# Performance work log

Hardware: AMD Instinct MI355X
Metric: run time of the kernel (lower is better)

The kernel has to match this reference:

```python
import jax, jax.numpy as jnp
import numpy as np

INPUT_DIM = 66
OUTPUT_COUNT = 8192
NUM_PAIRS = 65536

def setup_inputs() -> dict:
    key = jax.random.key(0)
    k1, k2, k3, k4 = jax.random.split(key, 4)
    x = jax.random.normal(k1, (NUM_PAIRS, INPUT_DIM), dtype=jnp.float32)
    query = jax.random.normal(k2, (OUTPUT_COUNT, INPUT_DIM), dtype=jnp.float32)
    # nn.Linear(input_dim, input_dim): weight [out,in], bias [out]
    bound = 1.0 / np.sqrt(INPUT_DIM)
    Wk = jax.random.uniform(k3, (INPUT_DIM, INPUT_DIM), minval=-bound, maxval=bound, dtype=jnp.float32)
    bk = jax.random.uniform(k4, (INPUT_DIM,), minval=-bound, maxval=bound, dtype=jnp.float32)
    return {"x": x, "query": query, "Wk": Wk, "bk": bk}

def reference(x, query, Wk, bk):
    # K = Linear(x): x @ Wk^T + bk  -> [num_pairs, d]
    K = x @ Wk.T + bk
    # scores: [output_count, num_pairs]
    scores = jnp.einsum("qd,nd->qn", query, K)
    attn = jax.nn.softmax(scores, axis=1)
    # selected: [output_count, d] — note values are raw x, not K
    selected = attn @ x
    return selected
```

## Files before the change

kernel.cpp:

```cpp
#include <hip/hip_runtime.h>
#include <cstdint>


typedef __bf16    bf16x4 __attribute__((ext_vector_type(4)));
typedef __bf16    bf16x8 __attribute__((ext_vector_type(8)));
typedef _Float16  f16x4  __attribute__((ext_vector_type(4)));
typedef _Float16  f16x8  __attribute__((ext_vector_type(8)));
typedef float     f32x16 __attribute__((ext_vector_type(16)));

extern "C" __device__ float __ocml_native_exp2_f32(float);

#define NUM_PAIRS   65536
#define NUM_Q       8192
#define DIM         66
#define KPITCH      84
#define QPITCH      80
#define XROWS       96
#define XPITCH      36
#define XTILE       (XROWS*XPITCH)
#define PARTP       68

#define LDS_XT 10752
#define STG    24576
#define KSTRIDE 10752
#define XSTRIDE 13824

__device__ __forceinline__ bf16x8 frag8(const __bf16* p) {
    bf16x4 lo = *(const bf16x4*)p;
    bf16x4 hi = *(const bf16x4*)(p + 4);
    return __builtin_shufflevector(lo, hi, 0, 1, 2, 3, 4, 5, 6, 7);
}
__device__ __forceinline__ f16x8 frag8h(const _Float16* p) {
    f16x4 lo = *(const f16x4*)p;
    f16x4 hi = *(const f16x4*)(p + 4);
    return __builtin_shufflevector(lo, hi, 0, 1, 2, 3, 4, 5, 6, 7);
}
__device__ __forceinline__ f32x16 mfma_bf16(bf16x8 a, bf16x8 b, f32x16 c) {
    return __builtin_amdgcn_mfma_f32_32x32x16_bf16(a, b, c, 0, 0, 0);
}
__device__ __forceinline__ f32x16 mfma_f16(f16x8 a, f16x8 b, f32x16 c) {
    return __builtin_amdgcn_mfma_f32_32x32x16_f16(a, b, c, 0, 0, 0);
}

__device__ __forceinline__ void plswap(unsigned &a, unsigned &b) {
    asm("v_permlane32_swap_b32 %0, %1" : "+v"(a), "+v"(b));
}
__device__ __forceinline__ unsigned packbf(float a, float b) {
    union { __bf16 h[2]; unsigned u; } t;
    t.h[0] = (__bf16)a; t.h[1] = (__bf16)b;
    return t.u;
}

union U4 { unsigned u[4]; bf16x8 v; };

__device__ __forceinline__ void makefrags(const f32x16 &s, U4 *f) {
    float P[16];
    #pragma unroll
    for (int r = 0; r < 16; ++r) P[r] = __ocml_native_exp2_f32(s[r]);
    unsigned E0 = packbf(P[0],  P[1]),  E1 = packbf(P[2],  P[3]);
    unsigned F0 = packbf(P[4],  P[5]),  F1 = packbf(P[6],  P[7]);
    plswap(E0, F0); plswap(E1, F1);
    f[0].u[0] = E0; f[0].u[1] = E1; f[0].u[2] = F0; f[0].u[3] = F1;
    unsigned G0 = packbf(P[8],  P[9]),  G1 = packbf(P[10], P[11]);
    unsigned H0 = packbf(P[12], P[13]), H1 = packbf(P[14], P[15]);
    plswap(G0, H0); plswap(G1, H1);
    f[1].u[0] = G0; f[1].u[1] = G1; f[1].u[2] = H0; f[1].u[3] = H1;
}

__device__ __forceinline__ void stage_tile(char* dst, const char* gK, const char* gX,
                                           int wave, int lane) {
    #pragma unroll
    for (int j = 0; j < 6; ++j) {
        int c = wave + 4 * j;
        int off = c * 1024 + lane * 16;
        const char* src = (off < KSTRIDE) ? (gK + off) : (gX + (off - KSTRIDE));
        __builtin_amdgcn_global_load_lds(
            (const __attribute__((address_space(1))) void*)(uintptr_t)src,
            (__attribute__((address_space(3))) void*)(unsigned int)(uintptr_t)(dst + c * 1024),
            16, 0, 0);
    }
}

__device__ __forceinline__ void compute_tile(const char* sm, const f16x8 (&aQ)[2][5],
                                             f32x16 (&o)[2][3], int l31, int h) {
    const _Float16* Kt = (const _Float16*)sm;
    const __bf16*   Xt = (const __bf16*)(sm + LDS_XT);
    #pragma unroll
    for (int pt = 0; pt < 2; ++pt) {
        f16x8 bK[5];
        #pragma unroll
        for (int kk = 0; kk < 5; ++kk)
            bK[kk] = frag8h(&Kt[(pt * 32 + l31) * KPITCH + kk * 16 + h * 8]);
        f32x16 s0 = {}, s1 = {};
        #pragma unroll
        for (int kk = 0; kk < 5; ++kk) {
            s0 = mfma_f16(bK[kk], aQ[0][kk], s0);
            s1 = mfma_f16(bK[kk], aQ[1][kk], s1);
        }
        U4 f[2][2];
        makefrags(s0, f[0]);
        makefrags(s1, f[1]);
        #pragma unroll
        for (int par = 0; par < 2; ++par) {
            const int kc = par * 16 + h * 8;
            #pragma unroll
            for (int dt = 0; dt < 3; ++dt) {
                bf16x8 bX = frag8(&Xt[pt * XTILE + (dt * 32 + l31) * XPITCH + kc]);
                o[0][dt] = mfma_bf16(f[0][par].v, bX, o[0][dt]);
                o[1][dt] = mfma_bf16(f[1][par].v, bX, o[1][dt]);
            }
        }
    }
}

#define PA_ROWS 128
#define PAP 104
__global__ __launch_bounds__(256) void prepA_kernel(
    const float* __restrict__ x, const float* __restrict__ Wk,
    const float* __restrict__ bk,
    unsigned short* __restrict__ Kh_u, unsigned short* __restrict__ Xb_u) {
    _Float16* Kh = (_Float16*)Kh_u;
    __bf16*   Xb = (__bf16*)Xb_u;
    __shared__ _Float16 sxh[PA_ROWS * PAP];
    __shared__ _Float16 sW[96 * PAP];
    const int tid = threadIdx.x;
    const long n0 = (long)blockIdx.x * PA_ROWS;

    for (int i = tid; i < PA_ROWS * 96; i += 256) {
        int r = i / 96, c = i % 96;
        sxh[r * PAP + c] = (_Float16)((c < DIM) ? x[(n0 + r) * DIM + c] : 0.f);
    }
    for (int i = tid; i < 96 * 96; i += 256) {
        int cc = i / 96, d = i % 96;
        sW[cc * PAP + d] = (_Float16)((cc < DIM && d < DIM) ? Wk[cc * DIM + d] : 0.f);
    }
    __syncthreads();

    const int lane = tid & 63, w = tid >> 6;
    const int l31 = lane & 31, h = lane >> 5;

    #pragma unroll
    for (int nt = 0; nt < 3; ++nt) {
        f32x16 acc = {};
        #pragma unroll
        for (int kk = 0; kk < 6; ++kk) {
            f16x8 a = *(const f16x8*)&sxh[(w * 32 + l31) * PAP + kk * 16 + h * 8];
            f16x8 b = *(const f16x8*)&sW[(nt * 32 + l31) * PAP + kk * 16 + h * 8];
            acc = mfma_f16(a, b, acc);
        }
        int c = nt * 32 + l31;
        float bkv = (c < DIM) ? bk[c] : 0.f;
        if (c < KPITCH) {
            #pragma unroll
            for (int r = 0; r < 16; ++r) {
                int row = (r & 3) + 8 * (r >> 2) + 4 * h;
                Kh[(n0 + w * 32 + row) * KPITCH + c] = (_Float16)(acc[r] + bkv);
            }
        }
    }

    for (int ii = tid; ii < 4 * XTILE; ii += 256) {
        int b = ii / XTILE, i = ii % XTILE;
        int dd = i / XPITCH, j = i % XPITCH;
        float v = 0.f;
        if (j < 32) {
            if (dd < DIM) v = (float)sxh[(b * 32 + j) * PAP + dd];
            else if (dd == DIM) v = 1.f;
        }
        Xb[((long)blockIdx.x * 4 + b) * XTILE + i] = (__bf16)v;
    }
}

__global__ __launch_bounds__(256) void prepB_kernel(
    const float* __restrict__ query, unsigned short* __restrict__ Qh_u) {
    _Float16* Qh = (_Float16*)Qh_u;
    int idx = blockIdx.x * 256 + threadIdx.x;
    int q = idx / QPITCH, c = idx % QPITCH;
    float v = (c < DIM) ? query[(long)q * DIM + c] * 1.4426950408889634f : 0.f;
    Qh[idx] = (_Float16)v;
}

__global__ __launch_bounds__(256, 2) void flash_kernel(
    const unsigned short* __restrict__ Qh_u, const unsigned short* __restrict__ Kh_u,
    const unsigned short* __restrict__ Xb_u, float* __restrict__ Part, int NS) {
    __shared__ __attribute__((aligned(16))) char smA[STG];
    __shared__ __attribute__((aligned(16))) char smB[STG];
    const _Float16* Qh = (const _Float16*)Qh_u;

    const int tid = threadIdx.x;
    const int lane = tid & 63, wave = tid >> 6;
    const int l31 = lane & 31, h = lane >> 5;
    const int qb = blockIdx.x / NS, ns = blockIdx.x % NS;
    const int ppc = NUM_PAIRS / NS;
    const int iters = ppc >> 6;
    const int qbase = qb * 256 + wave * 64;

    const long pbase = (long)ns * ppc;
    const char* gK0 = (const char*)Kh_u + pbase * (KPITCH * 2);
    const char* gX0 = (const char*)Xb_u + (pbase >> 5) * (XTILE * 2);

    f16x8 aQ[2][5];
    #pragma unroll
    for (int qt = 0; qt < 2; ++qt)
        #pragma unroll
        for (int kk = 0; kk < 5; ++kk)
            aQ[qt][kk] = *(const f16x8*)&Qh[(long)(qbase + qt * 32 + l31) * QPITCH + kk * 16 + h * 8];

    f32x16 o[2][3] = {};

    stage_tile(smA, gK0, gX0, wave, lane);
    for (int it = 0; it < iters; it += 2) {
        __syncthreads();
        if (it + 1 < iters)
            stage_tile(smB, gK0 + (long)(it + 1) * KSTRIDE,
                            gX0 + (long)(it + 1) * XSTRIDE, wave, lane);
        compute_tile(smA, aQ, o, l31, h);
        __syncthreads();
        if (it + 2 < iters)
            stage_tile(smA, gK0 + (long)(it + 2) * KSTRIDE,
                            gX0 + (long)(it + 2) * XSTRIDE, wave, lane);
        compute_tile(smB, aQ, o, l31, h);
    }

    float* dst = Part + (long)ns * NUM_Q * PARTP;
    #pragma unroll
    for (int qt = 0; qt < 2; ++qt)
        #pragma unroll
        for (int dt = 0; dt < 3; ++dt)
            #pragma unroll
            for (int r = 0; r < 16; ++r) {
                int row = (r & 3) + 8 * (r >> 2) + 4 * h;
                int q = qbase + qt * 32 + row;
                int d = dt * 32 + l31;
                if (d < DIM + 1) dst[(long)q * PARTP + d] = o[qt][dt][r];
            }
}

__global__ __launch_bounds__(256) void combine_kernel(
    const float* __restrict__ Part, float* __restrict__ out, int NS) {
    int q = blockIdx.x * 2 + (threadIdx.x >> 7);
    int d = threadIdx.x & 127;
    if (d >= DIM) return;
    float num = 0.f, den = 0.f;
    #pragma unroll 4
    for (int s = 0; s < NS; ++s) {
        const float* p = Part + ((long)s * NUM_Q + q) * PARTP;
        num += p[d];
        den += p[DIM];
    }
    out[(long)q * DIM + d] = num / den;
}

extern "C" void kernel_launch(void* const* d_in, const int* in_sizes, int n_in,
                              void* d_out, int out_size, void* d_ws, size_t ws_size,
                              hipStream_t stream) {
    const float* x     = (const float*)d_in[0];
    const float* query = (const float*)d_in[1];
    const float* Wk    = (const float*)d_in[2];
    const float* bk    = (const float*)d_in[3];
    float* out = (float*)d_out;
    char* ws = (char*)d_ws;

    unsigned short* Qh = (unsigned short*)(ws + 0);
    unsigned short* Kh = (unsigned short*)(ws + 1310720);
    unsigned short* Xb = (unsigned short*)(ws + 12320768);
    float* Part        = (float*)(ws + 26476544);

    int NS = 16;
    while (NS > 1 &&
           26476544ULL + (unsigned long long)NS * NUM_Q * PARTP * 4ULL > (unsigned long long)ws_size)
        NS >>= 1;

    prepA_kernel<<<NUM_PAIRS / PA_ROWS, 256, 0, stream>>>(x, Wk, bk, Kh, Xb);
    prepB_kernel<<<(NUM_Q * QPITCH) / 256, 256, 0, stream>>>(query, Qh);
    flash_kernel<<<(NUM_Q / 256) * NS, 256, 0, stream>>>(Qh, Kh, Xb, Part, NS);
    combine_kernel<<<NUM_Q / 2, 256, 0, stream>>>(Part, out, NS);
}
```

Measured before the change: 289.6 us.

## Halve flash tile to 32 queries per wave and merge prep kernels

The flash kernel now works on 32 queries per wave and 32 pairs per stage instead of 64×64. This halves LDS staging buffers and registers so four blocks can fit per CU, and it doubles the grid. The query conversion is folded into the prep kernel as extra blocks, which removes one launch. In exchange, each K/X tile loaded into LDS is reused across half as many queries, so total LDS and global traffic per output doubles.

```diff
diff --git a/kernel.cpp b/kernel.cpp
--- a/kernel.cpp
+++ b/kernel.cpp
@@ -20,10 +20,10 @@
 #define XTILE       (XROWS*XPITCH)
 #define PARTP       68
 
-#define LDS_XT 10752
-#define STG    24576
-#define KSTRIDE 10752
-#define XSTRIDE 13824
+#define LDS_XT 5376
+#define STG     12288
+#define KSTRIDE 5376
+#define XSTRIDE 6912
 
 __device__ __forceinline__ bf16x8 frag8(const __bf16* p) {
     bf16x4 lo = *(const bf16x4*)p;
@@ -70,7 +70,7 @@
 __device__ __forceinline__ void stage_tile(char* dst, const char* gK, const char* gX,
                                            int wave, int lane) {
     #pragma unroll
-    for (int j = 0; j < 6; ++j) {
+    for (int j = 0; j < 3; ++j) {
         int c = wave + 4 * j;
         int off = c * 1024 + lane * 16;
         const char* src = (off < KSTRIDE) ? (gK + off) : (gX + (off - KSTRIDE));
@@ -81,49 +81,54 @@
     }
 }
 
-__device__ __forceinline__ void compute_tile(const char* sm, const f16x8 (&aQ)[2][5],
-                                             f32x16 (&o)[2][3], int l31, int h) {
+__device__ __forceinline__ void compute_tile(const char* sm, const f16x8 (&aQ)[5],
+                                             f32x16 (&o)[3], int l31, int h) {
     const _Float16* Kt = (const _Float16*)sm;
     const __bf16*   Xt = (const __bf16*)(sm + LDS_XT);
-    #pragma unroll
-    for (int pt = 0; pt < 2; ++pt) {
-        f16x8 bK[5];
-        #pragma unroll
-        for (int kk = 0; kk < 5; ++kk)
-            bK[kk] = frag8h(&Kt[(pt * 32 + l31) * KPITCH + kk * 16 + h * 8]);
-        f32x16 s0 = {}, s1 = {};
-        #pragma unroll
-        for (int kk = 0; kk < 5; ++kk) {
-            s0 = mfma_f16(bK[kk], aQ[0][kk], s0);
-            s1 = mfma_f16(bK[kk], aQ[1][kk], s1);
-        }
-        U4 f[2][2];
-        makefrags(s0, f[0]);
-        makefrags(s1, f[1]);
-        #pragma unroll
-        for (int par = 0; par < 2; ++par) {
-            const int kc = par * 16 + h * 8;
-            #pragma unroll
-            for (int dt = 0; dt < 3; ++dt) {
-                bf16x8 bX = frag8(&Xt[pt * XTILE + (dt * 32 + l31) * XPITCH + kc]);
-                o[0][dt] = mfma_bf16(f[0][par].v, bX, o[0][dt]);
-                o[1][dt] = mfma_bf16(f[1][par].v, bX, o[1][dt]);
-            }
+    f16x8 bK[5];
+    #pragma unroll
+    for (int kk = 0; kk < 5; ++kk)
+        bK[kk] = frag8h(&Kt[l31 * KPITCH + kk * 16 + h * 8]);
+    f32x16 s = {};
+    #pragma unroll
+    for (int kk = 0; kk < 5; ++kk) s = mfma_f16(bK[kk], aQ[kk], s);
+    U4 f[2];
+    makefrags(s, f);
+    #pragma unroll
+    for (int par = 0; par < 2; ++par) {
+        const int kc = par * 16 + h * 8;
+        #pragma unroll
+        for (int dt = 0; dt < 3; ++dt) {
+            bf16x8 bX = frag8(&Xt[(dt * 32 + l31) * XPITCH + kc]);
+            o[dt] = mfma_bf16(f[par].v, bX, o[dt]);
         }
     }
 }
 
 #define PA_ROWS 128
 #define PAP 104
-__global__ __launch_bounds__(256) void prepA_kernel(
-    const float* __restrict__ x, const float* __restrict__ Wk,
-    const float* __restrict__ bk,
-    unsigned short* __restrict__ Kh_u, unsigned short* __restrict__ Xb_u) {
+__global__ __launch_bounds__(256) void prep_kernel(
+    const float* __restrict__ x, const float* __restrict__ query,
+    const float* __restrict__ Wk, const float* __restrict__ bk,
+    unsigned short* __restrict__ Kh_u, unsigned short* __restrict__ Xb_u,
+    unsigned short* __restrict__ Qh_u) {
+    const int tid = threadIdx.x;
+    if (blockIdx.x >= 512) {
+        _Float16* Qh = (_Float16*)Qh_u;
+        int base = (blockIdx.x - 512) * 1280;
+        #pragma unroll
+        for (int k = 0; k < 5; ++k) {
+            int idx = base + k * 256 + tid;
+            int q = idx / QPITCH, c = idx % QPITCH;
+            float v = (c < DIM) ? query[(long)q * DIM + c] * 1.4426950408889634f : 0.f;
+            Qh[idx] = (_Float16)v;
+        }
+        return;
+    }
     _Float16* Kh = (_Float16*)Kh_u;
     __bf16*   Xb = (__bf16*)Xb_u;
     __shared__ _Float16 sxh[PA_ROWS * PAP];
     __shared__ _Float16 sW[96 * PAP];
-    const int tid = threadIdx.x;
     const long n0 = (long)blockIdx.x * PA_ROWS;
 
     for (int i = tid; i < PA_ROWS * 96; i += 256) {
@@ -171,16 +176,7 @@
     }
 }
 
-__global__ __launch_bounds__(256) void prepB_kernel(
-    const float* __restrict__ query, unsigned short* __restrict__ Qh_u) {
-    _Float16* Qh = (_Float16*)Qh_u;
-    int idx = blockIdx.x * 256 + threadIdx.x;
-    int q = idx / QPITCH, c = idx % QPITCH;
-    float v = (c < DIM) ? query[(long)q * DIM + c] * 1.4426950408889634f : 0.f;
-    Qh[idx] = (_Float16)v;
-}
-
-__global__ __launch_bounds__(256, 2) void flash_kernel(
+__global__ __launch_bounds__(256, 4) void flash_kernel(
     const unsigned short* __restrict__ Qh_u, const unsigned short* __restrict__ Kh_u,
     const unsigned short* __restrict__ Xb_u, float* __restrict__ Part, int NS) {
     __shared__ __attribute__((aligned(16))) char smA[STG];
@@ -192,21 +188,19 @@
     const int l31 = lane & 31, h = lane >> 5;
     const int qb = blockIdx.x / NS, ns = blockIdx.x % NS;
     const int ppc = NUM_PAIRS / NS;
-    const int iters = ppc >> 6;
-    const int qbase = qb * 256 + wave * 64;
+    const int iters = ppc >> 5;
+    const int qbase = qb * 128 + wave * 32;
 
     const long pbase = (long)ns * ppc;
     const char* gK0 = (const char*)Kh_u + pbase * (KPITCH * 2);
     const char* gX0 = (const char*)Xb_u + (pbase >> 5) * (XTILE * 2);
 
-    f16x8 aQ[2][5];
-    #pragma unroll
-    for (int qt = 0; qt < 2; ++qt)
-        #pragma unroll
-        for (int kk = 0; kk < 5; ++kk)
-            aQ[qt][kk] = *(const f16x8*)&Qh[(long)(qbase + qt * 32 + l31) * QPITCH + kk * 16 + h * 8];
-
-    f32x16 o[2][3] = {};
+    f16x8 aQ[5];
+    #pragma unroll
+    for (int kk = 0; kk < 5; ++kk)
+        aQ[kk] = *(const f16x8*)&Qh[(long)(qbase + l31) * QPITCH + kk * 16 + h * 8];
+
+    f32x16 o[3] = {};
 
     stage_tile(smA, gK0, gX0, wave, lane);
     for (int it = 0; it < iters; it += 2) {
@@ -224,16 +218,14 @@
 
     float* dst = Part + (long)ns * NUM_Q * PARTP;
     #pragma unroll
-    for (int qt = 0; qt < 2; ++qt)
-        #pragma unroll
-        for (int dt = 0; dt < 3; ++dt)
-            #pragma unroll
-            for (int r = 0; r < 16; ++r) {
-                int row = (r & 3) + 8 * (r >> 2) + 4 * h;
-                int q = qbase + qt * 32 + row;
-                int d = dt * 32 + l31;
-                if (d < DIM + 1) dst[(long)q * PARTP + d] = o[qt][dt][r];
-            }
+    for (int dt = 0; dt < 3; ++dt)
+        #pragma unroll
+        for (int r = 0; r < 16; ++r) {
+            int row = (r & 3) + 8 * (r >> 2) + 4 * h;
+            int q = qbase + row;
+            int d = dt * 32 + l31;
+            if (d < DIM + 1) dst[(long)q * PARTP + d] = o[dt][r];
+        }
 }
 
 __global__ __launch_bounds__(256) void combine_kernel(
@@ -271,8 +263,7 @@
            26476544ULL + (unsigned long long)NS * NUM_Q * PARTP * 4ULL > (unsigned long long)ws_size)
         NS >>= 1;
 
-    prepA_kernel<<<NUM_PAIRS / PA_ROWS, 256, 0, stream>>>(x, Wk, bk, Kh, Xb);
-    prepB_kernel<<<(NUM_Q * QPITCH) / 256, 256, 0, stream>>>(query, Qh);
-    flash_kernel<<<(NUM_Q / 256) * NS, 256, 0, stream>>>(Qh, Kh, Xb, Part, NS);
+    prep_kernel<<<1024, 256, 0, stream>>>(x, query, Wk, bk, Kh, Xb, Qh);
+    flash_kernel<<<(NUM_Q / 128) * NS, 256, 0, stream>>>(Qh, Kh, Xb, Part, NS);
     combine_kernel<<<NUM_Q / 2, 256, 0, stream>>>(Part, out, NS);
 }
```

Measured after the change: 305.2 us. +5.4%, slower.
